# Performance work log

Hardware: AMD Instinct MI355X
Metric: run time of the kernel (lower is better)

Reference implementation:

```python
import jax, jax.numpy as jnp
import numpy as np

COMMITMENT_COST = 0.25
NUM_EMBEDDINGS = 8192
EMBEDDING_DIM = 64


def setup_inputs() -> dict:
    key = jax.random.key(0)
    k1, k2 = jax.random.split(key)
    z_e = jax.random.normal(k1, (32, 1024, EMBEDDING_DIM), dtype=jnp.float32)
    # nn.Embedding init: uniform(-1/num_embeddings, 1/num_embeddings)
    lim = 1.0 / NUM_EMBEDDINGS
    weight = jax.random.uniform(k2, (NUM_EMBEDDINGS, EMBEDDING_DIM), dtype=jnp.float32,
                                minval=-lim, maxval=lim)
    return {"z_e": z_e, "weight": weight}


def reference(z_e, weight):
    B = z_e.shape[0]
    D = weight.shape[1]
    z_flat = z_e.reshape(-1, D)  # [T, D], T = B*N
    # squared euclidean distances: ||z||^2 + ||e||^2 - 2 z e^T  -> [T, K]
    distances = (jnp.sum(z_flat ** 2, axis=1, keepdims=True)
                 + jnp.sum(weight ** 2, axis=1)
                 - 2.0 * jnp.matmul(z_flat, weight.T))
    encoding_indices = jnp.argmin(distances, axis=1)  # [T]
    # direct gather == one-hot @ weight (same math, no dense one-hot)
    z_q = weight[encoding_indices].reshape(z_e.shape)
    loss_1 = jnp.mean((jax.lax.stop_gradient(z_e) - z_q) ** 2)
    loss_2 = jnp.mean((z_e - jax.lax.stop_gradient(z_q)) ** 2)
    vq_loss = loss_1 + COMMITMENT_COST * loss_2
    # straight-through estimator
    z_q_st = z_e + jax.lax.stop_gradient(z_q - z_e)
    return (z_q_st, vq_loss)
```

## Files before the change

kernel.cpp:

```cpp
#include <hip/hip_runtime.h>

typedef float f32x16 __attribute__((ext_vector_type(16)));
typedef int v8i __attribute__((ext_vector_type(8)));

#define NUM_EMB 8192
#define DIM 64
#define NTOK 32768
#define TOKS_PER_BLOCK 32
#define TOK_BLOCKS 1024
#define WAVES 8
#define CHUNKS_PER_WAVE 32

#define B_SCALE (-8192.0f)
#define SCORE_BIAS 128.0f

__device__ __forceinline__ unsigned umin2(unsigned a, unsigned b) { return a < b ? a : b; }

__global__ __launch_bounds__(256) void vq_prep(const float* __restrict__ weight,
                                               uint4* __restrict__ wsB,
                                               float* __restrict__ loss_out) {
  int m = blockIdx.x * 256 + threadIdx.x;
  if (m == 0)
    __hip_atomic_store(loss_out, 0.0f, __ATOMIC_RELAXED, __HIP_MEMORY_SCOPE_AGENT);
  int lane = m & 63, h = (m >> 6) & 1, c = m >> 7;
  int n = c * 32 + (lane & 31);
  int kb = (lane >> 5) * 8;
  const float* p = weight + n * DIM;
  unsigned r[4];
#pragma unroll
  for (int q = 0; q < 2; ++q) {
    const float* pk = p + (2 * h + q) * 16 + kb;
    int lo = __builtin_amdgcn_cvt_pk_fp8_f32(B_SCALE * pk[0], B_SCALE * pk[1], 0, false);
    lo     = __builtin_amdgcn_cvt_pk_fp8_f32(B_SCALE * pk[2], B_SCALE * pk[3], lo, true);
    int hi = __builtin_amdgcn_cvt_pk_fp8_f32(B_SCALE * pk[4], B_SCALE * pk[5], 0, false);
    hi     = __builtin_amdgcn_cvt_pk_fp8_f32(B_SCALE * pk[6], B_SCALE * pk[7], hi, true);
    r[q * 2] = (unsigned)lo; r[q * 2 + 1] = (unsigned)hi;
  }
  wsB[m] = make_uint4(r[0], r[1], r[2], r[3]);
}

__global__ __launch_bounds__(512) void vq_main(const float* __restrict__ z_e,
                                               const float* __restrict__ weight,
                                               const uint4* __restrict__ wsB,
                                               float* __restrict__ out,
                                               float* __restrict__ loss_out) {
  __shared__ unsigned char lds_a[TOKS_PER_BLOCK * 72];
  __shared__ unsigned lds_part[WAVES][TOKS_PER_BLOCK];
  __shared__ unsigned lds_tok[TOKS_PER_BLOCK];
  __shared__ float wsum[WAVES];

  const int tid  = threadIdx.x;
  const int lane = tid & 63;
  const int wv   = tid >> 6;
  const int half = lane >> 5;
  const int ln31 = lane & 31;
  const int tbase = blockIdx.x * TOKS_PER_BLOCK;

  {
    int token = tid >> 4, q4 = tid & 15;
    const float* p = z_e + (size_t)(tbase + token) * DIM + q4 * 4;
    float4 x = *reinterpret_cast<const float4*>(p);
    int v = __builtin_amdgcn_cvt_pk_fp8_f32(x.x, x.y, 0, false);
    v     = __builtin_amdgcn_cvt_pk_fp8_f32(x.z, x.w, v, true);
    *reinterpret_cast<unsigned*>(&lds_a[token * 72 + q4 * 4]) = (unsigned)v;
  }
  __syncthreads();

  v8i a8;
  {
    union { uint2 d2[4]; v8i v; } au;
#pragma unroll
    for (int f = 0; f < 4; ++f)
      au.d2[f] = *reinterpret_cast<const uint2*>(&lds_a[ln31 * 72 + f * 16 + half * 8]);
    a8 = au.v;
  }

  f32x16 bias;
#pragma unroll
  for (int i = 0; i < 16; ++i) bias[i] = SCORE_BIAS;

  unsigned run[16];
#pragma unroll
  for (int i = 0; i < 16; ++i) run[i] = 0xFFFFFFFFu;

  const int c0 = wv * CHUNKS_PER_WAVE;
  unsigned idx = (unsigned)(c0 * 32 + ln31);

  uint4 bufA[2], bufB[2];
  bufA[0] = wsB[(c0 + 0) * 128 + lane];
  bufB[0] = wsB[(c0 + 0) * 128 + 64 + lane];
  bufA[1] = wsB[(c0 + 1) * 128 + lane];
  bufB[1] = wsB[(c0 + 1) * 128 + 64 + lane];

#pragma unroll 2
  for (int c = 0; c < CHUNKS_PER_WAVE; ++c) {
    uint4 curA = bufA[c & 1], curB = bufB[c & 1];
    int cn = c0 + c + 2;
    bufA[c & 1] = wsB[cn * 128 + lane];
    bufB[c & 1] = wsB[cn * 128 + 64 + lane];

    union { uint4 q[2]; v8i v; } bu;
    bu.q[0] = curA; bu.q[1] = curB;

    f32x16 acc = __builtin_amdgcn_mfma_scale_f32_32x32x64_f8f6f4(
        a8, bu.v, bias, 0 , 0 , 0, 0x7F, 0, 0x7F);

#pragma unroll
    for (int i = 0; i < 16; ++i)
      run[i] = umin2(run[i], (__float_as_uint(acc[i]) & 0xFFFFE000u) | idx);
    idx += 32;
  }

#pragma unroll
  for (int i = 0; i < 16; ++i) {
    unsigned v = run[i];
    v = umin2(v, (unsigned)__builtin_amdgcn_ds_swizzle((int)v, 0x041F));
    v = umin2(v, (unsigned)__builtin_amdgcn_ds_swizzle((int)v, 0x081F));
    v = umin2(v, (unsigned)__builtin_amdgcn_ds_swizzle((int)v, 0x101F));
    v = umin2(v, (unsigned)__builtin_amdgcn_ds_swizzle((int)v, 0x201F));
    v = umin2(v, (unsigned)__builtin_amdgcn_ds_swizzle((int)v, 0x401F));
    run[i] = v;
  }

  if (ln31 == 0) {
#pragma unroll
    for (int reg = 0; reg < 16; ++reg) {
      int row = (reg & 3) + 8 * (reg >> 2) + 4 * half;
      lds_part[wv][row] = run[reg];
    }
  }
  __syncthreads();

  if (tid < TOKS_PER_BLOCK) {
    unsigned k = lds_part[0][tid];
#pragma unroll
    for (int w = 1; w < WAVES; ++w) k = umin2(k, lds_part[w][tid]);
    lds_tok[tid] = k & 0x1FFFu;
  }
  __syncthreads();

  {
    int g = tid;
    int t = g >> 4, q = g & 15;
    float4 z = reinterpret_cast<const float4*>(z_e)[(size_t)tbase * 16 + g];
    float4 w = reinterpret_cast<const float4*>(weight)[(size_t)lds_tok[t] * 16 + q];
    float4 o;
    o.x = z.x + (w.x - z.x); o.y = z.y + (w.y - z.y);
    o.z = z.z + (w.z - z.z); o.w = z.w + (w.w - z.w);
    reinterpret_cast<float4*>(out)[(size_t)tbase * 16 + g] = o;
    float dx = z.x - w.x, dy = z.y - w.y, dz = z.z - w.z, dw = z.w - w.w;
    float lsum = dx * dx + dy * dy + dz * dz + dw * dw;
#pragma unroll
    for (int s = 32; s >= 1; s >>= 1) lsum += __shfl_xor(lsum, s, 64);
    if (lane == 0) wsum[wv] = lsum;
  }
  __syncthreads();
  if (tid == 0) {
    float tot = 0.0f;
#pragma unroll
    for (int i = 0; i < WAVES; ++i) tot += wsum[i];
    atomicAdd(loss_out, tot * (1.25f / 2097152.0f));
  }
}

extern "C" void kernel_launch(void* const* d_in, const int* in_sizes, int n_in,
                              void* d_out, int out_size, void* d_ws, size_t ws_size,
                              hipStream_t stream) {
  const float* z_e    = (const float*)d_in[0];
  const float* weight = (const float*)d_in[1];
  float* out  = (float*)d_out;
  float* loss = out + (out_size - 1);
  uint4* wsB = (uint4*)d_ws;

  vq_prep<<<128, 256, 0, stream>>>(weight, wsB, loss);
  vq_main<<<TOK_BLOCKS, 512, 0, stream>>>(z_e, weight, wsB, out, loss);
}
```

Baseline: 91.03 us.

## Process 64 tokens per block, reusing each codebook fragment for two MFMAs

Each block now handles 64 tokens instead of 32. Every wave keeps two A fragments and issues two MFMAs per loaded codebook chunk, so the fp8 codebook is streamed from memory half as often across the grid. The cost is double the running-min registers (run0/run1) and double the swizzle reduction work per wave, with a launch-bounds hint of 4 added to keep occupancy. The grid shrinks to 512 blocks, which may lower parallelism on a large GPU.

```diff
diff --git a/kernel.cpp b/kernel.cpp
--- a/kernel.cpp
+++ b/kernel.cpp
@@ -6,8 +6,8 @@
 #define NUM_EMB 8192
 #define DIM 64
 #define NTOK 32768
-#define TOKS_PER_BLOCK 32
-#define TOK_BLOCKS 1024
+#define TOKS_PER_BLOCK 64
+#define TOK_BLOCKS 512
 #define WAVES 8
 #define CHUNKS_PER_WAVE 32
 
@@ -39,11 +39,11 @@
   wsB[m] = make_uint4(r[0], r[1], r[2], r[3]);
 }
 
-__global__ __launch_bounds__(512) void vq_main(const float* __restrict__ z_e,
-                                               const float* __restrict__ weight,
-                                               const uint4* __restrict__ wsB,
-                                               float* __restrict__ out,
-                                               float* __restrict__ loss_out) {
+__global__ __launch_bounds__(512, 4) void vq_main(const float* __restrict__ z_e,
+                                                  const float* __restrict__ weight,
+                                                  const uint4* __restrict__ wsB,
+                                                  float* __restrict__ out,
+                                                  float* __restrict__ loss_out) {
   __shared__ unsigned char lds_a[TOKS_PER_BLOCK * 72];
   __shared__ unsigned lds_part[WAVES][TOKS_PER_BLOCK];
   __shared__ unsigned lds_tok[TOKS_PER_BLOCK];
@@ -56,9 +56,11 @@
   const int ln31 = lane & 31;
   const int tbase = blockIdx.x * TOKS_PER_BLOCK;
 
-  {
-    int token = tid >> 4, q4 = tid & 15;
-    const float* p = z_e + (size_t)(tbase + token) * DIM + q4 * 4;
+#pragma unroll
+  for (int rep = 0; rep < 2; ++rep) {
+    int g = rep * 512 + tid;
+    int token = g >> 4, q4 = g & 15;
+    const float* p = z_e + (size_t)tbase * DIM + (size_t)g * 4;
     float4 x = *reinterpret_cast<const float4*>(p);
     int v = __builtin_amdgcn_cvt_pk_fp8_f32(x.x, x.y, 0, false);
     v     = __builtin_amdgcn_cvt_pk_fp8_f32(x.z, x.w, v, true);
@@ -66,22 +68,24 @@
   }
   __syncthreads();
 
-  v8i a8;
-  {
+  v8i a8[2];
+#pragma unroll
+  for (int tg = 0; tg < 2; ++tg) {
     union { uint2 d2[4]; v8i v; } au;
 #pragma unroll
     for (int f = 0; f < 4; ++f)
-      au.d2[f] = *reinterpret_cast<const uint2*>(&lds_a[ln31 * 72 + f * 16 + half * 8]);
-    a8 = au.v;
+      au.d2[f] = *reinterpret_cast<const uint2*>(
+          &lds_a[(tg * 32 + ln31) * 72 + f * 16 + half * 8]);
+    a8[tg] = au.v;
   }
 
   f32x16 bias;
 #pragma unroll
   for (int i = 0; i < 16; ++i) bias[i] = SCORE_BIAS;
 
-  unsigned run[16];
+  unsigned run0[16], run1[16];
 #pragma unroll
-  for (int i = 0; i < 16; ++i) run[i] = 0xFFFFFFFFu;
+  for (int i = 0; i < 16; ++i) { run0[i] = 0xFFFFFFFFu; run1[i] = 0xFFFFFFFFu; }
 
   const int c0 = wv * CHUNKS_PER_WAVE;
   unsigned idx = (unsigned)(c0 * 32 + ln31);
@@ -102,31 +106,44 @@
     union { uint4 q[2]; v8i v; } bu;
     bu.q[0] = curA; bu.q[1] = curB;
 
-    f32x16 acc = __builtin_amdgcn_mfma_scale_f32_32x32x64_f8f6f4(
-        a8, bu.v, bias, 0 , 0 , 0, 0x7F, 0, 0x7F);
+    f32x16 acc0 = __builtin_amdgcn_mfma_scale_f32_32x32x64_f8f6f4(
+        a8[0], bu.v, bias, 0 , 0 , 0, 0x7F, 0, 0x7F);
+    f32x16 acc1 = __builtin_amdgcn_mfma_scale_f32_32x32x64_f8f6f4(
+        a8[1], bu.v, bias, 0, 0, 0, 0x7F, 0, 0x7F);
 
 #pragma unroll
     for (int i = 0; i < 16; ++i)
-      run[i] = umin2(run[i], (__float_as_uint(acc[i]) & 0xFFFFE000u) | idx);
+      run0[i] = umin2(run0[i], (__float_as_uint(acc0[i]) & 0xFFFFE000u) | idx);
+#pragma unroll
+    for (int i = 0; i < 16; ++i)
+      run1[i] = umin2(run1[i], (__float_as_uint(acc1[i]) & 0xFFFFE000u) | idx);
     idx += 32;
   }
 
 #pragma unroll
   for (int i = 0; i < 16; ++i) {
-    unsigned v = run[i];
+    unsigned v = run0[i];
     v = umin2(v, (unsigned)__builtin_amdgcn_ds_swizzle((int)v, 0x041F));
     v = umin2(v, (unsigned)__builtin_amdgcn_ds_swizzle((int)v, 0x081F));
     v = umin2(v, (unsigned)__builtin_amdgcn_ds_swizzle((int)v, 0x101F));
     v = umin2(v, (unsigned)__builtin_amdgcn_ds_swizzle((int)v, 0x201F));
     v = umin2(v, (unsigned)__builtin_amdgcn_ds_swizzle((int)v, 0x401F));
-    run[i] = v;
+    run0[i] = v;
+    unsigned w = run1[i];
+    w = umin2(w, (unsigned)__builtin_amdgcn_ds_swizzle((int)w, 0x041F));
+    w = umin2(w, (unsigned)__builtin_amdgcn_ds_swizzle((int)w, 0x081F));
+    w = umin2(w, (unsigned)__builtin_amdgcn_ds_swizzle((int)w, 0x101F));
+    w = umin2(w, (unsigned)__builtin_amdgcn_ds_swizzle((int)w, 0x201F));
+    w = umin2(w, (unsigned)__builtin_amdgcn_ds_swizzle((int)w, 0x401F));
+    run1[i] = w;
   }
 
   if (ln31 == 0) {
 #pragma unroll
     for (int reg = 0; reg < 16; ++reg) {
       int row = (reg & 3) + 8 * (reg >> 2) + 4 * half;
-      lds_part[wv][row] = run[reg];
+      lds_part[wv][row]      = run0[reg];
+      lds_part[wv][32 + row] = run1[reg];
     }
   }
   __syncthreads();
@@ -139,8 +156,10 @@
   }
   __syncthreads();
 
-  {
-    int g = tid;
+  float lsum = 0.0f;
+#pragma unroll
+  for (int rep = 0; rep < 2; ++rep) {
+    int g = rep * 512 + tid;
     int t = g >> 4, q = g & 15;
     float4 z = reinterpret_cast<const float4*>(z_e)[(size_t)tbase * 16 + g];
     float4 w = reinterpret_cast<const float4*>(weight)[(size_t)lds_tok[t] * 16 + q];
@@ -149,11 +168,11 @@
     o.z = z.z + (w.z - z.z); o.w = z.w + (w.w - z.w);
     reinterpret_cast<float4*>(out)[(size_t)tbase * 16 + g] = o;
     float dx = z.x - w.x, dy = z.y - w.y, dz = z.z - w.z, dw = z.w - w.w;
-    float lsum = dx * dx + dy * dy + dz * dz + dw * dw;
+    lsum += dx * dx + dy * dy + dz * dz + dw * dw;
+  }
 #pragma unroll
-    for (int s = 32; s >= 1; s >>= 1) lsum += __shfl_xor(lsum, s, 64);
-    if (lane == 0) wsum[wv] = lsum;
-  }
+  for (int s = 32; s >= 1; s >>= 1) lsum += __shfl_xor(lsum, s, 64);
+  if (lane == 0) wsum[wv] = lsum;
   __syncthreads();
   if (tid == 0) {
     float tot = 0.0f;
```

Result: slower. 133.4 us (+46.5%).

## Stage fp8 codebook in LDS via async global_load_lds and process 128 tokens per block

Applied to the files above, without the earlier changes.

Each block now handles 128 tokens instead of 32. Every wave owns 32 tokens and half of the codebook, so each B tile is reused by four waves. Codebook chunks are streamed into a double-buffered 64KB LDS area with global_load_lds, and one barrier per phase separates the 16 phases. This removes the 4x redundant per-wave global/L2 reads of the codebook, at the cost of more LDS traffic, a barrier per phase, fewer blocks (256), and lower occupancy from the large LDS footprint.

```diff
diff --git a/kernel.cpp b/kernel.cpp
--- a/kernel.cpp
+++ b/kernel.cpp
@@ -6,15 +6,23 @@
 #define NUM_EMB 8192
 #define DIM 64
 #define NTOK 32768
-#define TOKS_PER_BLOCK 32
-#define TOK_BLOCKS 1024
+#define TOKS_PER_BLOCK 128
+#define TOK_BLOCKS 256
 #define WAVES 8
-#define CHUNKS_PER_WAVE 32
+#define PHASES 16
+#define BUF_BYTES 32768
 
 #define B_SCALE (-8192.0f)
 #define SCORE_BIAS 128.0f
 
+#define AS1 __attribute__((address_space(1)))
+#define AS3 __attribute__((address_space(3)))
+
 __device__ __forceinline__ unsigned umin2(unsigned a, unsigned b) { return a < b ? a : b; }
+
+__device__ __forceinline__ void gload16(const void* g, void* l) {
+  __builtin_amdgcn_global_load_lds((const AS1 unsigned*)g, (AS3 unsigned*)l, 16, 0, 0);
+}
 
 __global__ __launch_bounds__(256) void vq_prep(const float* __restrict__ weight,
                                                uint4* __restrict__ wsB,
@@ -44,8 +52,9 @@
                                                const uint4* __restrict__ wsB,
                                                float* __restrict__ out,
                                                float* __restrict__ loss_out) {
-  __shared__ unsigned char lds_a[TOKS_PER_BLOCK * 72];
-  __shared__ unsigned lds_part[WAVES][TOKS_PER_BLOCK];
+  __shared__ __attribute__((aligned(16))) unsigned char lds_b[2 * BUF_BYTES];
+  __shared__ __attribute__((aligned(16))) unsigned char lds_a[TOKS_PER_BLOCK * 72];
+  __shared__ unsigned lds_part2[WAVES][32];
   __shared__ unsigned lds_tok[TOKS_PER_BLOCK];
   __shared__ float wsum[WAVES];
 
@@ -54,11 +63,23 @@
   const int wv   = tid >> 6;
   const int half = lane >> 5;
   const int ln31 = lane & 31;
+  const int eh   = wv >> 2;
+  const int wq   = wv & 3;
   const int tbase = blockIdx.x * TOKS_PER_BLOCK;
 
-  {
-    int token = tid >> 4, q4 = tid & 15;
-    const float* p = z_e + (size_t)(tbase + token) * DIM + q4 * 4;
+  const unsigned char* wsB8 = (const unsigned char*)wsB;
+  const size_t gslot = (size_t)eh * 262144u + (size_t)wq * 4096u + (size_t)lane * 16u;
+  const int lslot = eh * 16384 + wq * 4096;
+
+#pragma unroll
+  for (int r = 0; r < 4; ++r)
+    gload16(wsB8 + gslot + r * 1024, &lds_b[lslot + r * 1024]);
+
+#pragma unroll
+  for (int rep = 0; rep < 4; ++rep) {
+    int g = rep * 512 + tid;
+    int token = g >> 4, q4 = g & 15;
+    const float* p = z_e + (size_t)tbase * DIM + (size_t)g * 4;
     float4 x = *reinterpret_cast<const float4*>(p);
     int v = __builtin_amdgcn_cvt_pk_fp8_f32(x.x, x.y, 0, false);
     v     = __builtin_amdgcn_cvt_pk_fp8_f32(x.z, x.w, v, true);
@@ -71,7 +92,8 @@
     union { uint2 d2[4]; v8i v; } au;
 #pragma unroll
     for (int f = 0; f < 4; ++f)
-      au.d2[f] = *reinterpret_cast<const uint2*>(&lds_a[ln31 * 72 + f * 16 + half * 8]);
+      au.d2[f] = *reinterpret_cast<const uint2*>(
+          &lds_a[(wq * 32 + ln31) * 72 + f * 16 + half * 8]);
     a8 = au.v;
   }
 
@@ -83,32 +105,33 @@
 #pragma unroll
   for (int i = 0; i < 16; ++i) run[i] = 0xFFFFFFFFu;
 
-  const int c0 = wv * CHUNKS_PER_WAVE;
-  unsigned idx = (unsigned)(c0 * 32 + ln31);
-
-  uint4 bufA[2], bufB[2];
-  bufA[0] = wsB[(c0 + 0) * 128 + lane];
-  bufB[0] = wsB[(c0 + 0) * 128 + 64 + lane];
-  bufA[1] = wsB[(c0 + 1) * 128 + lane];
-  bufB[1] = wsB[(c0 + 1) * 128 + 64 + lane];
-
-#pragma unroll 2
-  for (int c = 0; c < CHUNKS_PER_WAVE; ++c) {
-    uint4 curA = bufA[c & 1], curB = bufB[c & 1];
-    int cn = c0 + c + 2;
-    bufA[c & 1] = wsB[cn * 128 + lane];
-    bufB[c & 1] = wsB[cn * 128 + 64 + lane];
-
-    union { uint4 q[2]; v8i v; } bu;
-    bu.q[0] = curA; bu.q[1] = curB;
-
-    f32x16 acc = __builtin_amdgcn_mfma_scale_f32_32x32x64_f8f6f4(
-        a8, bu.v, bias, 0 , 0 , 0, 0x7F, 0, 0x7F);
-
-#pragma unroll
-    for (int i = 0; i < 16; ++i)
-      run[i] = umin2(run[i], (__float_as_uint(acc[i]) & 0xFFFFE000u) | idx);
-    idx += 32;
+#pragma unroll 1
+  for (int p = 0; p < PHASES; ++p) {
+    const int cb = p & 1;
+    if (p + 1 < PHASES) {
+      const int nb = cb ^ 1;
+#pragma unroll
+      for (int r = 0; r < 4; ++r)
+        gload16(wsB8 + gslot + (size_t)(p + 1) * 16384 + r * 1024,
+                &lds_b[nb * BUF_BYTES + lslot + r * 1024]);
+    }
+    {
+      const unsigned char* lb = &lds_b[cb * BUF_BYTES + eh * 16384];
+      unsigned idx = (unsigned)((eh * 128 + p * 8) * 32 + ln31);
+#pragma unroll
+      for (int j = 0; j < 8; ++j) {
+        union { uint4 q[2]; v8i v; } bu;
+        bu.q[0] = *reinterpret_cast<const uint4*>(lb + j * 2048 + lane * 16);
+        bu.q[1] = *reinterpret_cast<const uint4*>(lb + j * 2048 + 1024 + lane * 16);
+        f32x16 acc = __builtin_amdgcn_mfma_scale_f32_32x32x64_f8f6f4(
+            a8, bu.v, bias, 0 , 0 , 0, 0x7F, 0, 0x7F);
+#pragma unroll
+        for (int i = 0; i < 16; ++i)
+          run[i] = umin2(run[i], (__float_as_uint(acc[i]) & 0xFFFFE000u) | idx);
+        idx += 32;
+      }
+    }
+    __syncthreads();
   }
 
 #pragma unroll
@@ -126,21 +149,22 @@
 #pragma unroll
     for (int reg = 0; reg < 16; ++reg) {
       int row = (reg & 3) + 8 * (reg >> 2) + 4 * half;
-      lds_part[wv][row] = run[reg];
+      lds_part2[wv][row] = run[reg];
     }
   }
   __syncthreads();
 
   if (tid < TOKS_PER_BLOCK) {
-    unsigned k = lds_part[0][tid];
-#pragma unroll
-    for (int w = 1; w < WAVES; ++w) k = umin2(k, lds_part[w][tid]);
+    int tg = tid >> 5, r = tid & 31;
+    unsigned k = umin2(lds_part2[tg][r], lds_part2[tg + 4][r]);
     lds_tok[tid] = k & 0x1FFFu;
   }
   __syncthreads();
 
-  {
-    int g = tid;
+  float lsum = 0.0f;
+#pragma unroll
+  for (int rep = 0; rep < 4; ++rep) {
+    int g = rep * 512 + tid;
     int t = g >> 4, q = g & 15;
     float4 z = reinterpret_cast<const float4*>(z_e)[(size_t)tbase * 16 + g];
     float4 w = reinterpret_cast<const float4*>(weight)[(size_t)lds_tok[t] * 16 + q];
@@ -149,11 +173,11 @@
     o.z = z.z + (w.z - z.z); o.w = z.w + (w.w - z.w);
     reinterpret_cast<float4*>(out)[(size_t)tbase * 16 + g] = o;
     float dx = z.x - w.x, dy = z.y - w.y, dz = z.z - w.z, dw = z.w - w.w;
-    float lsum = dx * dx + dy * dy + dz * dz + dw * dw;
-#pragma unroll
-    for (int s = 32; s >= 1; s >>= 1) lsum += __shfl_xor(lsum, s, 64);
-    if (lane == 0) wsum[wv] = lsum;
-  }
+    lsum += dx * dx + dy * dy + dz * dz + dw * dw;
+  }
+#pragma unroll
+  for (int s = 32; s >= 1; s >>= 1) lsum += __shfl_xor(lsum, s, 64);
+  if (lane == 0) wsum[wv] = lsum;
   __syncthreads();
   if (tid == 0) {
     float tot = 0.0f;
```

After: 97.33 us. 1.07x slower.
